# Optimization experiments

Hardware: AMD Instinct MI355X
Metric: run time of the kernel (lower is better)

The kernel has to match this reference:

```python
import jax, jax.numpy as jnp
import numpy as np

B, S, D, H, E = 2, 512, 768, 12, 8
FF = 4 * D
HD = D // H


def setup_inputs() -> dict:
    key = jax.random.key(0)
    ks = jax.random.split(key, 12)
    s = 0.02
    return {
        "x": jax.random.normal(ks[0], (B, S, D), jnp.float32),
        "ln1_g": jnp.ones((D,), jnp.float32),
        "ln1_b": jnp.zeros((D,), jnp.float32),
        "ln2_g": jnp.ones((D,), jnp.float32),
        "ln2_b": jnp.zeros((D,), jnp.float32),
        "in_proj_w": jax.random.normal(ks[1], (3 * D, D), jnp.float32) * s,
        "in_proj_b": jax.random.normal(ks[2], (3 * D,), jnp.float32) * s,
        "out_proj_w": jax.random.normal(ks[3], (D, D), jnp.float32) * s,
        "out_proj_b": jax.random.normal(ks[4], (D,), jnp.float32) * s,
        "router_w": jax.random.normal(ks[5], (E, D), jnp.float32) * s,
        "router_b": jax.random.normal(ks[6], (E,), jnp.float32) * s,
        "w1": jax.random.normal(ks[7], (E, D, FF), jnp.float32) * s,
        "b1": jax.random.normal(ks[8], (E, FF), jnp.float32) * s,
        "w2": jax.random.normal(ks[9], (E, FF, D), jnp.float32) * s,
        "b2": jax.random.normal(ks[10], (E, D), jnp.float32) * s,
    }


def _layernorm(x, g, b, eps=1e-5):
    mu = x.mean(-1, keepdims=True)
    var = ((x - mu) ** 2).mean(-1, keepdims=True)
    return (x - mu) * jax.lax.rsqrt(var + eps) * g + b


def _forward(x, ln1_g, ln1_b, ln2_g, ln2_b, in_proj_w, in_proj_b,
             out_proj_w, out_proj_b, router_w, router_b, w1, b1, w2, b2):
    # --- self-attention sublayer (pre-norm per torch module ordering) ---
    h = _layernorm(x, ln1_g, ln1_b)
    qkv = h @ in_proj_w.T + in_proj_b                     # [B,S,3D]
    q, k, v = jnp.split(qkv, 3, axis=-1)
    to_heads = lambda t: t.reshape(B, S, H, HD).transpose(0, 2, 1, 3)  # [B,H,S,hd]
    q, k, v = to_heads(q), to_heads(k), to_heads(v)
    scores = jnp.einsum('bhqd,bhkd->bhqk', q, k) / np.float32(np.sqrt(HD))
    attn = jax.nn.softmax(scores, axis=-1)
    o = jnp.einsum('bhqk,bhkd->bhqd', attn, v).transpose(0, 2, 1, 3).reshape(B, S, D)
    o = o @ out_proj_w.T + out_proj_b
    x = x + o
    # --- MoE sublayer: top-2 routing, renormalized gates ---
    h2 = _layernorm(x, ln2_g, ln2_b)
    t = h2.reshape(-1, D)                                  # [T,D]
    logits = t @ router_w.T + router_b                     # [T,E]
    probs = jax.nn.softmax(logits, axis=-1)
    top_v, top_i = jax.lax.top_k(probs, 2)                 # [T,2]
    top_v = top_v / top_v.sum(-1, keepdims=True)
    # per-(token, expert) combine weight (0 if expert not in token's top-2)
    comb = jnp.sum(jax.nn.one_hot(top_i, E, dtype=probs.dtype) * top_v[..., None], axis=1)  # [T,E]
    # dense grouped-FFN: every token through every expert, zero-weighted combine
    hid = jax.nn.gelu(jnp.einsum('td,edf->tef', t, w1) + b1, approximate=False)  # exact GELU as torch
    y = jnp.einsum('tef,efd->ted', hid, w2) + b2           # [T,E,D]
    moe = jnp.einsum('te,ted->td', comb, y).reshape(B, S, D)
    return x + moe


def reference(x, ln1_g, ln1_b, ln2_g, ln2_b, in_proj_w, in_proj_b,
              out_proj_w, out_proj_b, router_w, router_b, w1, b1, w2, b2):
    return _forward(x, ln1_g, ln1_b, ln2_g, ln2_b, in_proj_w, in_proj_b,
                    out_proj_w, out_proj_b, router_w, router_b, w1, b1, w2, b2)
```

## Files before the change

### kernel.cpp

```cpp
#include <hip/hip_runtime.h>
#include <hip/hip_bf16.h>

#define BATCH 2
#define SEQ 512
#define DIM 768
#define HEADS 12
#define NEXP 8
#define FFDIM 3072
#define HDIM 64
#define NTOK (BATCH*SEQ)
#define NENT (2*NTOK)
#define YPS ((long)NENT * DIM)

typedef __hip_bfloat16 bf16;
typedef __attribute__((ext_vector_type(8))) short s8v;
typedef __attribute__((ext_vector_type(4))) float f4v;

typedef __attribute__((address_space(1))) const unsigned char gas_u8;
typedef __attribute__((address_space(3))) unsigned char las_u8;
__device__ __forceinline__ void gload16(const void* g, void* l) {
    __builtin_amdgcn_global_load_lds((gas_u8*)g, (las_u8*)l, 16, 0, 0);
}

__device__ __forceinline__ float bfbits2f(unsigned hi16) {
    union { unsigned u; float f; } c; c.u = hi16; return c.f;
}
__device__ __forceinline__ unsigned short bf16bits(float f) {
    bf16 h = __float2bfloat16(f);
    return *reinterpret_cast<unsigned short*>(&h);
}

__global__ __launch_bounds__(256) void ln_kernel(const float* __restrict__ x,
                                                 const float* __restrict__ g,
                                                 const float* __restrict__ b,
                                                 bf16* __restrict__ outb) {
    int t = blockIdx.x;
    const float* xr = x + (long)t * DIM;
    int tid = threadIdx.x;
    float v0 = xr[tid], v1 = xr[tid + 256], v2 = xr[tid + 512];
    float s = v0 + v1 + v2;
    __shared__ float red[4];
    #pragma unroll
    for (int o = 32; o; o >>= 1) s += __shfl_xor(s, o);
    if ((tid & 63) == 0) red[tid >> 6] = s;
    __syncthreads();
    s = red[0] + red[1] + red[2] + red[3];
    float mu = s * (1.f / DIM);
    float d0 = v0 - mu, d1 = v1 - mu, d2 = v2 - mu;
    float q = d0*d0 + d1*d1 + d2*d2;
    __shared__ float red2[4];
    #pragma unroll
    for (int o = 32; o; o >>= 1) q += __shfl_xor(q, o);
    if ((tid & 63) == 0) red2[tid >> 6] = q;
    __syncthreads();
    q = red2[0] + red2[1] + red2[2] + red2[3];
    float rstd = rsqrtf(q * (1.f / DIM) + 1e-5f);
    bf16* ob = outb + (long)t * DIM;
    ob[tid]       = __float2bfloat16(d0 * rstd * g[tid]       + b[tid]);
    ob[tid + 256] = __float2bfloat16(d1 * rstd * g[tid + 256] + b[tid + 256]);
    ob[tid + 512] = __float2bfloat16(d2 * rstd * g[tid + 512] + b[tid + 512]);
}

__global__ __launch_bounds__(256) void ln2x1_kernel(const float* __restrict__ x,
                                                    const float* __restrict__ out_b,
                                                    const float* __restrict__ op,
                                                    const float* __restrict__ g,
                                                    const float* __restrict__ b,
                                                    float* __restrict__ x1,
                                                    float* __restrict__ t2,
                                                    bf16* __restrict__ t2b) {
    int t = blockIdx.x;
    long base = (long)t * DIM;
    int tid = threadIdx.x;
    const long TDl = (long)NTOK * DIM;
    float v[3];
    #pragma unroll
    for (int i = 0; i < 3; ++i) {
        long idx = base + tid + i * 256;
        v[i] = x[idx] + out_b[tid + i * 256] + op[idx] + op[idx + TDl];
        x1[idx] = v[i];
    }
    float s = v[0] + v[1] + v[2];
    __shared__ float red[4];
    #pragma unroll
    for (int o = 32; o; o >>= 1) s += __shfl_xor(s, o);
    if ((tid & 63) == 0) red[tid >> 6] = s;
    __syncthreads();
    s = red[0] + red[1] + red[2] + red[3];
    float mu = s * (1.f / DIM);
    float d[3];
    float q = 0.f;
    #pragma unroll
    for (int i = 0; i < 3; ++i) { d[i] = v[i] - mu; q += d[i] * d[i]; }
    __shared__ float red2[4];
    #pragma unroll
    for (int o = 32; o; o >>= 1) q += __shfl_xor(q, o);
    if ((tid & 63) == 0) red2[tid >> 6] = q;
    __syncthreads();
    q = red2[0] + red2[1] + red2[2] + red2[3];
    float rstd = rsqrtf(q * (1.f / DIM) + 1e-5f);
    #pragma unroll
    for (int i = 0; i < 3; ++i) {
        long idx = base + tid + i * 256;
        float o = d[i] * rstd * g[tid + i * 256] + b[tid + i * 256];
        t2[idx] = o;
        t2b[idx] = __float2bfloat16(o);
    }
}

template<int WM, int WN, bool GROUPED, bool GELU, int OUTMODE>
__global__ __launch_bounds__(256) void mfma_gemm(
    const bf16* __restrict__ A, const bf16* __restrict__ B,
    const float* __restrict__ bias, const float* __restrict__ resid,
    void* __restrict__ Cv,
    int M, int N, int K, int lda, int ldb, int ldc,
    int zdiv, int ksplit,
    long a_hi, long a_lo, long b_hi, long b_lo, long c_hi, long c_lo,
    long bias_stride, const int* __restrict__ grp_off, float alpha)
{
    constexpr int BM = 32 * WM, BN = 32 * WN;
    constexpr int ACH = BM * 4;
    constexpr int BCH = BN * 4;

    int z = blockIdx.z;
    int ze = z / ksplit, ks = z % ksplit;
    int kper = K / ksplit;
    long aoff, boff, coff;
    int m_count = M;
    if (GROUPED) {
        int m0 = grp_off[ze], m1 = grp_off[ze + 1];
        m_count = m1 - m0;
        if ((int)blockIdx.y * BM >= m_count) return;
        aoff = (long)m0 * lda;
        coff = (long)m0 * ldc;
        boff = (long)ze * b_hi;
    } else {
        int zh = ze / zdiv, zl = ze % zdiv;
        aoff = zh * a_hi + zl * a_lo;
        boff = zh * b_hi + zl * b_lo;
        coff = zh * c_hi + zl * c_lo;
    }
    const short* Ag = (const short*)(A + aoff);
    const short* Bg = (const short*)(B + boff);
    const float* biasp = bias ? bias + (long)ze * bias_stride : nullptr;
    float* Cf = (float*)Cv + coff;
    bf16*  Cb = (bf16*)Cv + coff;

    __shared__ short As[BM * 32];
    __shared__ short Bs[BN * 32];

    int tid = threadIdx.x;
    int wv = tid >> 6, ln = tid & 63;
    int wr = wv >> 1, wc = wv & 1;
    int fr = ln & 15, fq = ln >> 4;
    int bm = blockIdx.y * BM, bn = blockIdx.x * BN;

    f4v acc[WM][WN] = {};

    for (int k0 = ks * kper; k0 < (ks + 1) * kper; k0 += 32) {
        #pragma unroll
        for (int is = 0; is < ACH / 256; ++is) {
            int c = is * 256 + wv * 64 + ln;
            int m = c >> 2, kq = c & 3;
            int qg = kq ^ ((m >> 1) & 3);
            gload16(Ag + (long)(bm + m) * lda + k0 + qg * 8,
                    &As[(is * 256 + wv * 64) * 8]);
        }
        if constexpr (ACH % 256) {
            if (tid < ACH % 256) {
                int c = (ACH / 256) * 256 + tid;
                int m = c >> 2, kq = c & 3;
                int qg = kq ^ ((m >> 1) & 3);
                gload16(Ag + (long)(bm + m) * lda + k0 + qg * 8,
                        &As[((ACH / 256) * 256 + wv * 64) * 8]);
            }
        }
        #pragma unroll
        for (int is = 0; is < BCH / 256; ++is) {
            int c = is * 256 + wv * 64 + ln;
            int m = c >> 2, kq = c & 3;
            int qg = kq ^ ((m >> 1) & 3);
            gload16(Bg + (long)(bn + m) * ldb + k0 + qg * 8,
                    &Bs[(is * 256 + wv * 64) * 8]);
        }
        if constexpr (BCH % 256) {
            if (tid < BCH % 256) {
                int c = (BCH / 256) * 256 + tid;
                int m = c >> 2, kq = c & 3;
                int qg = kq ^ ((m >> 1) & 3);
                gload16(Bg + (long)(bn + m) * ldb + k0 + qg * 8,
                        &Bs[((BCH / 256) * 256 + wv * 64) * 8]);
            }
        }
        __syncthreads();
        s8v av[WM], bv[WN];
        #pragma unroll
        for (int i = 0; i < WM; ++i) {
            int row = wr * (WM * 16) + i * 16 + fr;
            av[i] = *(const s8v*)&As[row * 32 + (fq ^ ((row >> 1) & 3)) * 8];
        }
        #pragma unroll
        for (int j = 0; j < WN; ++j) {
            int row = wc * (WN * 16) + j * 16 + fr;
            bv[j] = *(const s8v*)&Bs[row * 32 + (fq ^ ((row >> 1) & 3)) * 8];
        }
        #pragma unroll
        for (int i = 0; i < WM; ++i)
            #pragma unroll
            for (int j = 0; j < WN; ++j)
                acc[i][j] = __builtin_amdgcn_mfma_f32_16x16x32_bf16(av[i], bv[j], acc[i][j], 0, 0, 0);
        __syncthreads();
    }

    #pragma unroll
    for (int i = 0; i < WM; ++i) {
        #pragma unroll
        for (int r = 0; r < 4; ++r) {
            int row = bm + wr * (WM * 16) + i * 16 + fq * 4 + r;
            if (GROUPED && row >= m_count) continue;
            #pragma unroll
            for (int j = 0; j < WN; ++j) {
                int col = bn + wc * (WN * 16) + j * 16 + fr;
                if (col < N) {
                    float v = acc[i][j][r] * alpha;
                    if (OUTMODE == 2) {
                        atomicAdd(&Cf[(long)row * ldc + col], v);
                    } else {
                        if (biasp) v += biasp[col];
                        if (GELU) v = 0.5f * v * (1.f + erff(v * 0.70710678118654752f));
                        if (resid) v += resid[(long)row * ldc + col];
                        if (OUTMODE == 1) Cb[(long)row * ldc + col] = __float2bfloat16(v);
                        else              Cf[(long)row * ldc + col] = v;
                    }
                }
            }
        }
    }
}

template<int FM, int FN, int XT, int YCAP, int KS, bool GELU, int OUTMODE, bool GATHER>
__global__ __launch_bounds__(256) void moe_gemm(
    const bf16* __restrict__ A, const bf16* __restrict__ B,
    const float* __restrict__ bias, void* __restrict__ Cv,
    int lda, int ldb, int ldc, int Ktot, long b_hi, long bias_stride,
    const int* __restrict__ grp_off, const int* __restrict__ entry_tok,
    int N, long pstride)
{
    static_assert(OUTMODE != 1 || KS == 1, "plain bf16 store requires no split-K");
    constexpr int BM = FM * 32, BN = FN * 32;
    constexpr int GA = BM / 64;
    constexpr int GB = BN / 64;
    constexpr int G = GA + GB;

    int bid = blockIdx.x;
    int e = bid & 7;
    int r = bid >> 3;
    int xt = r % XT; r /= XT;
    int yt = r % YCAP;
    int ks = r / YCAP;
    int m0 = grp_off[e], m1 = grp_off[e + 1];
    int m_count = m1 - m0;
    int bm = yt * BM;
    if (bm >= m_count) return;
    int bn = xt * BN;
    int kper = Ktot / KS;

    const short* Ag = (const short*)A + (GATHER ? 0 : (long)m0 * lda);
    const short* Bg = (const short*)(B + (long)e * b_hi);
    const float* biasp = bias ? bias + (long)e * bias_stride : nullptr;
    float* Cf = (float*)Cv + (long)m0 * ldc + (long)ks * pstride;
    bf16*  Cb = (bf16*)Cv + (long)m0 * ldc;

    __shared__ short As[3][BM * 32];
    __shared__ short Bs[3][BN * 32];

    int tid = threadIdx.x;
    int wv = tid >> 6, ln = tid & 63;
    int wr = wv >> 1, wc = wv & 1;
    int fr = ln & 15, fq = ln >> 4;

    long arow[GA];
    #pragma unroll
    for (int is = 0; is < GA; ++is) {
        int c = is * 256 + wv * 64 + ln;
        int m = c >> 2;
        if (GATHER) {
            int gi = m0 + bm + m;
            arow[is] = (long)entry_tok[gi < NENT ? gi : NENT - 1] * lda;
        } else {
            arow[is] = (long)(bm + m) * lda;
        }
    }

    f4v acc[FM][FN] = {};

    auto stage = [&](int buf, int k0) {
        #pragma unroll
        for (int is = 0; is < GA; ++is) {
            int c = is * 256 + wv * 64 + ln;
            int m = c >> 2, q = c & 3;
            int qg = q ^ ((m >> 1) & 3);
            gload16(Ag + arow[is] + k0 + qg * 8,
                    &As[buf][(is * 256 + wv * 64) * 8]);
        }
        #pragma unroll
        for (int is = 0; is < GB; ++is) {
            int c = is * 256 + wv * 64 + ln;
            int n = c >> 2, q = c & 3;
            int qg = q ^ ((n >> 1) & 3);
            gload16(Bg + (long)(bn + n) * ldb + k0 + qg * 8,
                    &Bs[buf][(is * 256 + wv * 64) * 8]);
        }
    };

    int kbeg = ks * kper;
    int nit = kper / 32;
    stage(0, kbeg);
    if (nit > 1) stage(1, kbeg + 32);

    for (int it = 0; it < nit; ++it) {
        if (it + 1 < nit) asm volatile("s_waitcnt vmcnt(%0)" :: "i"(G) : "memory");
        else              asm volatile("s_waitcnt vmcnt(0)" ::: "memory");
        __builtin_amdgcn_s_barrier();
        if (it + 2 < nit) stage((it + 2) % 3, kbeg + (it + 2) * 32);
        int cur = it % 3;
        __builtin_amdgcn_s_setprio(1);
        {
            s8v av[FM], bv[FN];
            #pragma unroll
            for (int i = 0; i < FM; ++i) {
                int row = wr * (FM * 16) + i * 16 + fr;
                av[i] = *(const s8v*)&As[cur][row * 32 + (fq ^ ((row >> 1) & 3)) * 8];
            }
            #pragma unroll
            for (int j = 0; j < FN; ++j) {
                int row = wc * (FN * 16) + j * 16 + fr;
                bv[j] = *(const s8v*)&Bs[cur][row * 32 + (fq ^ ((row >> 1) & 3)) * 8];
            }
            #pragma unroll
            for (int i = 0; i < FM; ++i)
                #pragma unroll
                for (int j = 0; j < FN; ++j)
                    acc[i][j] = __builtin_amdgcn_mfma_f32_16x16x32_bf16(av[i], bv[j], acc[i][j], 0, 0, 0);
        }
        __builtin_amdgcn_s_setprio(0);
    }

    #pragma unroll
    for (int i = 0; i < FM; ++i) {
        #pragma unroll
        for (int rr = 0; rr < 4; ++rr) {
            int row = bm + wr * (FM * 16) + i * 16 + fq * 4 + rr;
            if (row >= m_count) continue;
            #pragma unroll
            for (int j = 0; j < FN; ++j) {
                int col = bn + wc * (FN * 16) + j * 16 + fr;
                float v = acc[i][j][rr];
                if (OUTMODE == 0) {
                    Cf[(long)row * ldc + col] = v;
                } else {
                    if (biasp) v += biasp[col];
                    if (GELU) v = 0.5f * v * (1.f + erff(v * 0.70710678118654752f));
                    Cb[(long)row * ldc + col] = __float2bfloat16(v);
                }
            }
        }
    }
}

__global__ __launch_bounds__(256) void softmax512b(const bf16* __restrict__ s,
                                                   bf16* __restrict__ attn) {
    long row = (long)blockIdx.x * 4 + (threadIdx.x >> 6);
    int ln = threadIdx.x & 63;
    const unsigned* p = (const unsigned*)(s + row * 512);
    uint4 v = *(const uint4*)(p + ln * 4);
    unsigned u[4] = {v.x, v.y, v.z, v.w};
    float f[8];
    #pragma unroll
    for (int j = 0; j < 4; ++j) {
        f[2*j]   = bfbits2f(u[j] << 16);
        f[2*j+1] = bfbits2f(u[j] & 0xffff0000u);
    }
    float m = f[0];
    #pragma unroll
    for (int j = 1; j < 8; ++j) m = fmaxf(m, f[j]);
    #pragma unroll
    for (int o = 32; o; o >>= 1) m = fmaxf(m, __shfl_xor(m, o));
    float e[8], ssum = 0.f;
    #pragma unroll
    for (int j = 0; j < 8; ++j) { e[j] = expf(f[j] - m); ssum += e[j]; }
    #pragma unroll
    for (int o = 32; o; o >>= 1) ssum += __shfl_xor(ssum, o);
    float inv = 1.f / ssum;
    unsigned w[4];
    #pragma unroll
    for (int j = 0; j < 4; ++j) {
        bf16 lo = __float2bfloat16(e[2*j] * inv);
        bf16 hi = __float2bfloat16(e[2*j+1] * inv);
        w[j] = ((unsigned)*(unsigned short*)&hi << 16) | *(unsigned short*)&lo;
    }
    uint4 o4; o4.x = w[0]; o4.y = w[1]; o4.z = w[2]; o4.w = w[3];
    *(uint4*)((unsigned*)(attn + row * 512) + ln * 4) = o4;
}

__global__ __launch_bounds__(256) void vt_kernel(const bf16* __restrict__ qkvb,
                                                 bf16* __restrict__ vt) {
    int st = blockIdx.x;
    int z = blockIdx.y;
    int b = z / HEADS, h = z % HEADS;
    __shared__ short tile[64][65];
    int t = threadIdx.x;
    int d = t & 63, s0 = t >> 6;
    const short* q = (const short*)qkvb;
    #pragma unroll
    for (int i = 0; i < 16; ++i) {
        int s = st * 64 + s0 + i * 4;
        tile[s0 + i * 4][d] = q[(long)(b * SEQ + s) * 2304 + 2 * DIM + h * HDIM + d];
    }
    __syncthreads();
    short* o = (short*)vt;
    #pragma unroll
    for (int i = 0; i < 16; ++i) {
        int d2 = (t >> 6) + i * 4;
        o[(long)(z * 64 + d2) * 512 + st * 64 + (t & 63)] = tile[t & 63][d2];
    }
}

__global__ __launch_bounds__(256) void wtrans2_kernel(const float* __restrict__ w1,
                                                      bf16* __restrict__ w1t,
                                                      const float* __restrict__ w2,
                                                      bf16* __restrict__ w2t) {
    int id = blockIdx.x;
    const float* in; bf16* out; int R, C, e, ct, rt;
    if (id < 4608) {
        e = id / 576; int rem = id % 576; ct = rem / 12; rt = rem % 12;
        in = w1; out = w1t; R = DIM; C = FFDIM;
    } else {
        id -= 4608;
        e = id / 576; int rem = id % 576; ct = rem / 48; rt = rem % 48;
        in = w2; out = w2t; R = FFDIM; C = DIM;
    }
    long ibase = (long)e * R * C;
    int rt0 = rt * 64, ct0 = ct * 64;
    __shared__ float tile[64][65];
    int t = threadIdx.x;
    {
        int q = t >> 4, cq = t & 15;
        #pragma unroll
        for (int i = 0; i < 4; ++i) {
            int row = q + i * 16;
            float4 v = *(const float4*)&in[ibase + (long)(rt0 + row) * C + ct0 + cq * 4];
            tile[row][cq * 4]     = v.x;
            tile[row][cq * 4 + 1] = v.y;
            tile[row][cq * 4 + 2] = v.z;
            tile[row][cq * 4 + 3] = v.w;
        }
    }
    __syncthreads();
    {
        int q = t >> 4, rq = t & 15;
        #pragma unroll
        for (int i = 0; i < 4; ++i) {
            int cc = q + i * 16;
            unsigned lo = ((unsigned)bf16bits(tile[rq * 4 + 1][cc]) << 16) | bf16bits(tile[rq * 4][cc]);
            unsigned hi = ((unsigned)bf16bits(tile[rq * 4 + 3][cc]) << 16) | bf16bits(tile[rq * 4 + 2][cc]);
            uint2 u; u.x = lo; u.y = hi;
            *(uint2*)&out[ibase + (long)(ct0 + cc) * R + rt0 + rq * 4] = u;
        }
    }
}

__global__ __launch_bounds__(256) void cvt2_kernel(const float* __restrict__ a, long na,
                                                   const float* __restrict__ b, long nb,
                                                   bf16* __restrict__ oa,
                                                   bf16* __restrict__ ob) {
    long i = ((long)blockIdx.x * 256 + threadIdx.x) * 4;
    const float* src; bf16* dst; long idx;
    if (i < na) { src = a; dst = oa; idx = i; }
    else if (i < na + nb) { src = b; dst = ob; idx = i - na; }
    else return;
    float4 v = *(const float4*)(src + idx);
    dst[idx]     = __float2bfloat16(v.x);
    dst[idx + 1] = __float2bfloat16(v.y);
    dst[idx + 2] = __float2bfloat16(v.z);
    dst[idx + 3] = __float2bfloat16(v.w);
}

__global__ __launch_bounds__(64) void router_kernel(const float* __restrict__ t2,
                                                    const float* __restrict__ rw,
                                                    const float* __restrict__ rb,
                                                    int* __restrict__ e_sel,
                                                    float* __restrict__ w_sel) {
    int t = blockIdx.x;
    int lane = threadIdx.x;
    const float* tr = t2 + (long)t * DIM;
    float tv[12];
    #pragma unroll
    for (int i = 0; i < 12; ++i) tv[i] = tr[lane + 64 * i];
    float logits[NEXP];
    #pragma unroll
    for (int e = 0; e < NEXP; ++e) {
        const float* wr = rw + (long)e * DIM;
        float s = 0.f;
        #pragma unroll
        for (int i = 0; i < 12; ++i) s += tv[i] * wr[lane + 64 * i];
        #pragma unroll
        for (int o = 32; o; o >>= 1) s += __shfl_xor(s, o);
        logits[e] = s + rb[e];
    }
    if (lane == 0) {
        int e0 = -1, e1 = -1;
        float l0 = -1e30f, l1 = -1e30f;
        #pragma unroll
        for (int e = 0; e < NEXP; ++e) {
            float l = logits[e];
            if (l > l0) { l1 = l0; e1 = e0; l0 = l; e0 = e; }
            else if (l > l1) { l1 = l; e1 = e; }
        }
        float p1 = expf(l1 - l0);
        float inv = 1.f / (1.f + p1);
        e_sel[t * 2] = e0;  e_sel[t * 2 + 1] = e1;
        w_sel[t * 2] = inv; w_sel[t * 2 + 1] = p1 * inv;
    }
}

__global__ __launch_bounds__(1024) void build_lists(const int* __restrict__ e_sel,
                                                    int* __restrict__ entry_tok,
                                                    int* __restrict__ pos,
                                                    int* __restrict__ grp_off) {
    __shared__ int cnt[NEXP];
    __shared__ int off[NEXP + 1];
    __shared__ int cur[NEXP];
    int tid = threadIdx.x;
    if (tid < NEXP) cnt[tid] = 0;
    __syncthreads();
    for (int i = tid; i < NENT; i += 1024) atomicAdd(&cnt[e_sel[i]], 1);
    __syncthreads();
    if (tid == 0) {
        off[0] = 0;
        for (int e = 0; e < NEXP; ++e) off[e + 1] = off[e] + cnt[e];
        for (int e = 0; e < NEXP; ++e) cur[e] = off[e];
    }
    __syncthreads();
    for (int i = tid; i < NENT; i += 1024) {
        int e = e_sel[i];
        int p = atomicAdd(&cur[e], 1);
        entry_tok[p] = i >> 1;
        pos[i] = p;
    }
    if (tid < NEXP + 1) grp_off[tid] = off[tid];
}

__global__ __launch_bounds__(256) void combine_kernel(const float* __restrict__ x1,
                                                      const float* __restrict__ ypart,
                                                      const float* __restrict__ b2,
                                                      const int* __restrict__ pos,
                                                      const int* __restrict__ e_sel,
                                                      const float* __restrict__ wsel,
                                                      float* __restrict__ out) {
    long i4 = (long)blockIdx.x * 256 + threadIdx.x;
    if (i4 >= (long)NTOK * DIM / 4) return;
    int t = (int)(i4 / 192), d4 = (int)(i4 % 192);
    const float4* x1v = (const float4*)x1;
    const float4* ypv = (const float4*)ypart;
    const float4* b2v = (const float4*)b2;
    float4 v = x1v[i4];
    #pragma unroll
    for (int s = 0; s < 2; ++s) {
        long base = (long)pos[t * 2 + s] * 192 + d4;
        float4 y = b2v[(long)e_sel[t * 2 + s] * 192 + d4];
        #pragma unroll
        for (int ks = 0; ks < 4; ++ks) {
            float4 pp = ypv[base + ks * (YPS / 4)];
            y.x += pp.x; y.y += pp.y; y.z += pp.z; y.w += pp.w;
        }
        float w = wsel[t * 2 + s];
        v.x += w * y.x; v.y += w * y.y; v.z += w * y.z; v.w += w * y.w;
    }
    ((float4*)out)[i4] = v;
}

extern "C" void kernel_launch(void* const* d_in, const int* in_sizes, int n_in,
                              void* d_out, int out_size, void* d_ws, size_t ws_size,
                              hipStream_t stream) {
    const float* x        = (const float*)d_in[0];
    const float* ln1_g    = (const float*)d_in[1];
    const float* ln1_b    = (const float*)d_in[2];
    const float* ln2_g    = (const float*)d_in[3];
    const float* ln2_b    = (const float*)d_in[4];
    const float* in_w     = (const float*)d_in[5];
    const float* in_b     = (const float*)d_in[6];
    const float* out_w    = (const float*)d_in[7];
    const float* out_b    = (const float*)d_in[8];
    const float* router_w = (const float*)d_in[9];
    const float* router_b = (const float*)d_in[10];
    const float* w1       = (const float*)d_in[11];
    const float* b1       = (const float*)d_in[12];
    const float* w2       = (const float*)d_in[13];
    const float* b2       = (const float*)d_in[14];
    float* out = (float*)d_out;

    const long TD = (long)NTOK * DIM;
    char* p = (char*)d_ws;
    size_t off = 0;
    auto alloc = [&](size_t bytes) -> void* {
        void* r = p + off; off += (bytes + 255) & ~(size_t)255; return r;
    };
    bf16*  h_b    = (bf16*)alloc(TD * 2);
    bf16*  in_wb  = (bf16*)alloc(2304L * 768 * 2);
    bf16*  qkv_b  = (bf16*)alloc(1024L * 2304 * 2);
    bf16*  out_wb = (bf16*)alloc(768L * 768 * 2);
    bf16*  vt_b   = (bf16*)alloc((24L * 64 + 64) * 512 * 2);
    bf16*  oat_b  = (bf16*)alloc(TD * 2);
    float* opart  = (float*)alloc(2 * TD * 4);
    float* x1     = (float*)alloc(TD * 4);
    float* t2     = (float*)alloc(TD * 4);
    bf16*  t2b    = (bf16*)alloc((NTOK + 256L) * DIM * 2);
    bf16*  w1t    = (bf16*)alloc(8L * 3072 * 768 * 2);
    bf16*  w2t    = (bf16*)alloc(8L * 768 * 3072 * 2);
    bf16*  hid    = (bf16*)alloc((2048L + 256) * 3072 * 2);
    float* ypart  = (float*)alloc(4 * YPS * 4);
    int*   e_sel     = (int*)alloc(NENT * 4);
    float* w_sel     = (float*)alloc(NENT * 4);
    int*   entry_tok = (int*)alloc(NENT * 4);
    int*   pos       = (int*)alloc(NENT * 4);
    int*   grp_off   = (int*)alloc(64);
    bf16* scores = w1t;
    bf16* attn   = (bf16*)((char*)w1t + 24L * 512 * 512 * 2);

    ln_kernel<<<NTOK, 256, 0, stream>>>(x, ln1_g, ln1_b, h_b);
    cvt2_kernel<<<2304, 256, 0, stream>>>(in_w, 2304L * 768, out_w, 768L * 768,
                                          in_wb, out_wb);
    mfma_gemm<2, 2, false, false, 1><<<dim3(36, 16, 1), 256, 0, stream>>>(
        h_b, in_wb, in_b, nullptr, qkv_b,
        NTOK, 3 * DIM, DIM, DIM, DIM, 3 * DIM,
        1, 1, 0, 0, 0, 0, 0, 0, 0, nullptr, 1.f);
    mfma_gemm<2, 4, false, false, 1><<<dim3(4, 8, 24), 256, 0, stream>>>(
        qkv_b, qkv_b + DIM, nullptr, nullptr, scores,
        SEQ, SEQ, HDIM, 3 * DIM, 3 * DIM, SEQ,
        HEADS, 1, (long)SEQ * 3 * DIM, HDIM, (long)SEQ * 3 * DIM, HDIM,
        (long)HEADS * SEQ * SEQ, (long)SEQ * SEQ,
        0, nullptr, 0.125f);
    softmax512b<<<24 * SEQ / 4, 256, 0, stream>>>(scores, attn);
    vt_kernel<<<dim3(8, 24), 256, 0, stream>>>(qkv_b, vt_b);
    mfma_gemm<1, 2, false, false, 1><<<dim3(1, 16, 24), 256, 0, stream>>>(
        attn, vt_b, nullptr, nullptr, oat_b,
        SEQ, HDIM, SEQ, SEQ, SEQ, DIM,
        HEADS, 1, (long)HEADS * SEQ * SEQ, (long)SEQ * SEQ,
        (long)HEADS * HDIM * SEQ, (long)HDIM * SEQ,
        (long)SEQ * DIM, HDIM,
        0, nullptr, 1.f);
    mfma_gemm<2, 2, false, false, 0><<<dim3(12, 16, 2), 256, 0, stream>>>(
        oat_b, out_wb, nullptr, nullptr, opart,
        NTOK, DIM, 384, DIM, DIM, DIM,
        2, 1, 0, 384, 0, 384, 0, TD, 0, nullptr, 1.f);
    ln2x1_kernel<<<NTOK, 256, 0, stream>>>(x, out_b, opart, ln2_g, ln2_b,
                                           x1, t2, t2b);
    router_kernel<<<NTOK, 64, 0, stream>>>(t2, router_w, router_b, e_sel, w_sel);
    build_lists<<<1, 1024, 0, stream>>>(e_sel, entry_tok, pos, grp_off);
    wtrans2_kernel<<<9216, 256, 0, stream>>>(w1, w1t, w2, w2t);
    moe_gemm<4, 4, 24, 8, 1, true, 1, true><<<8 * 24 * 8, 256, 0, stream>>>(
        t2b, w1t, b1, hid,
        DIM, DIM, FFDIM, DIM, (long)FFDIM * DIM, FFDIM, grp_off, entry_tok,
        FFDIM, 0);
    moe_gemm<4, 4, 6, 8, 4, false, 0, false><<<8 * 6 * 8 * 4, 256, 0, stream>>>(
        hid, w2t, nullptr, ypart,
        FFDIM, FFDIM, DIM, FFDIM, (long)DIM * FFDIM, 0, grp_off, nullptr,
        DIM, YPS);
    combine_kernel<<<768, 256, 0, stream>>>(x1, ypart, b2, pos, e_sel, w_sel, out);
}
```

Baseline: 185.3 us.

## Store MoE expert weights in k-blocked layout for contiguous B-tile loads

Result: no change. 187.8 us (+1.4%).

```diff
diff --git a/kernel.cpp b/kernel.cpp
--- a/kernel.cpp
+++ b/kernel.cpp
@@ -242,7 +242,7 @@
 __global__ __launch_bounds__(256) void moe_gemm(
     const bf16* __restrict__ A, const bf16* __restrict__ B,
     const float* __restrict__ bias, void* __restrict__ Cv,
-    int lda, int ldb, int ldc, int Ktot, long b_hi, long bias_stride,
+    int lda, int Nt, int ldc, int Ktot, long b_hi, long bias_stride,
     const int* __restrict__ grp_off, const int* __restrict__ entry_tok,
     int N, long pstride)
 {
@@ -308,7 +308,7 @@
             int c = is * 256 + wv * 64 + ln;
             int n = c >> 2, q = c & 3;
             int qg = q ^ ((n >> 1) & 3);
-            gload16(Bg + (long)(bn + n) * ldb + k0 + qg * 8,
+            gload16(Bg + ((long)(k0 >> 3) + qg) * Nt * 8 + (long)(bn + n) * 8,
                     &Bs[buf][(is * 256 + wv * 64) * 8]);
         }
     };
@@ -431,16 +431,16 @@
                                                       const float* __restrict__ w2,
                                                       bf16* __restrict__ w2t) {
     int id = blockIdx.x;
-    const float* in; bf16* out; int R, C, e, ct, rt;
+    const float* in; bf16* out; int C, e, ct, rt;
     if (id < 4608) {
         e = id / 576; int rem = id % 576; ct = rem / 12; rt = rem % 12;
-        in = w1; out = w1t; R = DIM; C = FFDIM;
+        in = w1; out = w1t; C = FFDIM;
     } else {
         id -= 4608;
         e = id / 576; int rem = id % 576; ct = rem / 48; rt = rem % 48;
-        in = w2; out = w2t; R = FFDIM; C = DIM;
-    }
-    long ibase = (long)e * R * C;
+        in = w2; out = w2t; C = DIM;
+    }
+    long ibase = (long)e * DIM * FFDIM;
     int rt0 = rt * 64, ct0 = ct * 64;
     __shared__ float tile[64][65];
     int t = threadIdx.x;
@@ -458,14 +458,18 @@
     }
     __syncthreads();
     {
-        int q = t >> 4, rq = t & 15;
-        #pragma unroll
-        for (int i = 0; i < 4; ++i) {
-            int cc = q + i * 16;
-            unsigned lo = ((unsigned)bf16bits(tile[rq * 4 + 1][cc]) << 16) | bf16bits(tile[rq * 4][cc]);
-            unsigned hi = ((unsigned)bf16bits(tile[rq * 4 + 3][cc]) << 16) | bf16bits(tile[rq * 4 + 2][cc]);
-            uint2 u; u.x = lo; u.y = hi;
-            *(uint2*)&out[ibase + (long)(ct0 + cc) * R + rt0 + rq * 4] = u;
+        int kb2 = t >> 6, n = t & 63;
+        #pragma unroll
+        for (int i = 0; i < 2; ++i) {
+            int kblk = kb2 + 4 * i;
+            unsigned w[4];
+            #pragma unroll
+            for (int j = 0; j < 4; ++j) {
+                w[j] = ((unsigned)bf16bits(tile[kblk * 8 + 2 * j + 1][n]) << 16)
+                     | bf16bits(tile[kblk * 8 + 2 * j][n]);
+            }
+            uint4 u; u.x = w[0]; u.y = w[1]; u.z = w[2]; u.w = w[3];
+            *(uint4*)&out[ibase + ((long)(rt0 >> 3) + kblk) * C * 8 + (long)(ct0 + n) * 8] = u;
         }
     }
 }
@@ -661,11 +665,11 @@
     wtrans2_kernel<<<9216, 256, 0, stream>>>(w1, w1t, w2, w2t);
     moe_gemm<4, 4, 24, 8, 1, true, 1, true><<<8 * 24 * 8, 256, 0, stream>>>(
         t2b, w1t, b1, hid,
-        DIM, DIM, FFDIM, DIM, (long)FFDIM * DIM, FFDIM, grp_off, entry_tok,
+        DIM, FFDIM, FFDIM, DIM, (long)FFDIM * DIM, FFDIM, grp_off, entry_tok,
         FFDIM, 0);
     moe_gemm<4, 4, 6, 8, 4, false, 0, false><<<8 * 6 * 8 * 4, 256, 0, stream>>>(
         hid, w2t, nullptr, ypart,
-        FFDIM, FFDIM, DIM, FFDIM, (long)DIM * FFDIM, 0, grp_off, nullptr,
+        FFDIM, DIM, DIM, FFDIM, (long)FFDIM * DIM, 0, grp_off, nullptr,
         DIM, YPS);
     combine_kernel<<<768, 256, 0, stream>>>(x1, ypart, b2, pos, e_sel, w_sel, out);
 }
```
